# Optimization experiments

Measured on AMD Instinct MI355X. Metric: run time of the kernel, lower is better.

The kernel has to match this reference:

```python
import jax, jax.numpy as jnp
import numpy as np

NUM_EMBEDDINGS = 1024
EMBEDDING_SIZE = 256
COMMITMENT_COST = 0.25


def setup_inputs() -> dict:
    key = jax.random.key(0)
    kx, kw = jax.random.split(key)
    x = jax.random.normal(kx, (16, EMBEDDING_SIZE, 64, 64), dtype=jnp.float32)
    # nn.Embedding init: uniform(-1/K, 1/K)
    w = jax.random.uniform(kw, (NUM_EMBEDDINGS, EMBEDDING_SIZE), dtype=jnp.float32,
                           minval=-1.0 / NUM_EMBEDDINGS, maxval=1.0 / NUM_EMBEDDINGS)
    return {"x": x, "w": w}


def reference(x, w):
    # x: [B, C, H, W] -> NHWC
    xh = jnp.transpose(x, (0, 2, 3, 1))  # [B, H, W, D]
    B, H, W, D = xh.shape
    x_flat = xh.reshape(-1, D)  # [N, D]
    distances = (jnp.sum(x_flat * x_flat, axis=1, keepdims=True)
                 + jnp.sum(w * w, axis=1)
                 - 2.0 * (x_flat @ w.T))  # [N, K]
    indices_flat = jnp.argmin(distances, axis=1)  # [N]
    quantized = w[indices_flat].reshape(B, H, W, D)
    indices = indices_flat.reshape(B, H, W)[:, None, :, :]  # [B,1,H,W]
    # training-mode losses
    e_latent_loss = jnp.mean((jax.lax.stop_gradient(quantized) - xh) ** 2)
    q_latent_loss = jnp.mean((quantized - jax.lax.stop_gradient(xh)) ** 2)
    loss = q_latent_loss + COMMITMENT_COST * e_latent_loss
    # straight-through estimator
    quantized = xh + jax.lax.stop_gradient(quantized - xh)
    quantized = jnp.transpose(quantized, (0, 3, 1, 2))  # back to NCHW
    return quantized, indices, loss
```

## Files before the change

kernel.cpp:

```cpp
#include <hip/hip_runtime.h>
#include <math.h>

#define NUM_K 1024
#define DIM 256
#define HW 4096
#define NPIX 65536
#define QELEMS 16777216
#define MAX_FLAGS 16384

typedef short bf16x8 __attribute__((ext_vector_type(8)));
typedef float f32x4 __attribute__((ext_vector_type(4)));

__device__ __forceinline__ unsigned short f32_to_bf16_rne(float f) {
    unsigned int u = __float_as_uint(f);
    unsigned int r = u + 0x7FFFu + ((u >> 16) & 1u);
    return (unsigned short)(r >> 16);
}
__device__ __forceinline__ float bf16_to_f32(unsigned short h) {
    return __uint_as_float(((unsigned int)h) << 16);
}

__device__ __forceinline__ void merge3(float& a1d, int& a1i, float& a2d, int& a2i, float& a3d,
                                       float b1d, int b1i, float b2d, int b2i, float b3d) {
    bool bf = (b1d < a1d) || (b1d == a1d && b1i < a1i);
    float r1d = bf ? b1d : a1d; int r1i = bf ? b1i : a1i;
    float n2d = bf ? b2d : a2d; int n2i = bf ? b2i : a2i;
    float o1d = bf ? a1d : b1d; int o1i = bf ? a1i : b1i;
    bool k2 = (n2d < o1d) || (n2d == o1d && n2i < o1i);
    float r2d = k2 ? n2d : o1d; int r2i = k2 ? n2i : o1i;
    float sm3 = bf ? b3d : a3d;
    float o2d = bf ? a2d : b2d;
    float r3d = k2 ? fminf(sm3, o1d) : fminf(n2d, o2d);
    a1d = r1d; a1i = r1i; a2d = r2d; a2i = r2i; a3d = r3d;
}

__device__ __forceinline__ float np_sumsq_256(const float* __restrict__ p, long stride) {
    float blk0 = 0.f, blk1 = 0.f;
#pragma unroll
    for (int h = 0; h < 2; ++h) {
        const float* base = p + (long)h * 128 * stride;
        float s[16];
#pragma unroll
        for (int L = 0; L < 16; ++L) {
            float a0 = base[(long)(L)       * stride]; a0 = __fmul_rn(a0, a0);
            float a1 = base[(long)(16 + L)  * stride]; a1 = __fmul_rn(a1, a1);
            float a2 = base[(long)(32 + L)  * stride]; a2 = __fmul_rn(a2, a2);
            float a3 = base[(long)(48 + L)  * stride]; a3 = __fmul_rn(a3, a3);
            float a4 = base[(long)(64 + L)  * stride]; a4 = __fmul_rn(a4, a4);
            float a5 = base[(long)(80 + L)  * stride]; a5 = __fmul_rn(a5, a5);
            float a6 = base[(long)(96 + L)  * stride]; a6 = __fmul_rn(a6, a6);
            float a7 = base[(long)(112 + L) * stride]; a7 = __fmul_rn(a7, a7);
            float t1 = __fadd_rn(a0, a1);
            float t2 = __fadd_rn(a2, a3);
            float t3 = __fadd_rn(a4, a5);
            float t4 = __fadd_rn(a6, a7);
            s[L] = __fadd_rn(__fadd_rn(t1, t2), __fadd_rn(t3, t4));
        }
        float c0 = __fadd_rn(s[0], s[8]);
        float c1 = __fadd_rn(s[1], s[9]);
        float c2 = __fadd_rn(s[2], s[10]);
        float c3 = __fadd_rn(s[3], s[11]);
        float c4 = __fadd_rn(s[4], s[12]);
        float c5 = __fadd_rn(s[5], s[13]);
        float c6 = __fadd_rn(s[6], s[14]);
        float c7 = __fadd_rn(s[7], s[15]);
        float d0 = __fadd_rn(c0, c4);
        float d1 = __fadd_rn(c1, c5);
        float d2 = __fadd_rn(c2, c6);
        float d3 = __fadd_rn(c3, c7);
        float e0 = __fadd_rn(d0, d2);
        float e1 = __fadd_rn(d1, d3);
        float r  = __fadd_rn(e0, e1);
        if (h == 0) blk0 = r; else blk1 = r;
    }
    return __fadd_rn(blk0, blk1);
}

__global__ __launch_bounds__(256) void k_wsq(const float* __restrict__ w, float* __restrict__ wsq) {
    int k = blockIdx.x * 256 + threadIdx.x;
    if (k < NUM_K) wsq[k] = np_sumsq_256(w + (long)k * DIM, 1);
}

__global__ __launch_bounds__(256) void k_xsq(const float* __restrict__ x, float* __restrict__ xsq) {
    int n = blockIdx.x * 256 + threadIdx.x;
    int b = n >> 12, hw = n & 4095;
    xsq[n] = np_sumsq_256(x + (long)b * DIM * HW + hw, HW);
}

__global__ __launch_bounds__(1024)
void k_wtrans(const float* __restrict__ w, float* __restrict__ wtr) {
    int d = blockIdx.x;
    int k = threadIdx.x;
    wtr[(long)d * NUM_K + k] = w[(long)k * DIM + d];
}

__global__ __launch_bounds__(256)
void k_wfrag(const float* __restrict__ w, short* __restrict__ whi) {
    int id = blockIdx.x * 256 + threadIdx.x;
    int code = id >> 5;
    int c = id & 31;
    const float* src = w + (long)code * DIM + c * 8;
    bf16x8 vh;
#pragma unroll
    for (int j = 0; j < 8; ++j) vh[j] = (short)f32_to_bf16_rne(src[j]);
    int fl = ((c & 3) << 4) | (code & 15);
    long addr = ((((long)(code >> 4) * 8 + (c >> 2)) * 64 + fl) * 8);
    *(bf16x8*)(whi + addr) = vh;
}

#define A_SLOT(ks,m,fl) ((((ks)*4+(m))*64+(fl))*8)

__global__ __launch_bounds__(256, 2)
void k_argmin_mfma(const float* __restrict__ x,
                   const short* __restrict__ whi,
                   const float* __restrict__ wsq, const float* __restrict__ xsq,
                   float* __restrict__ pd1, int* __restrict__ pi1,
                   float* __restrict__ pd2, int* __restrict__ pi2,
                   float* __restrict__ pd3) {
    __shared__ short ahi[8 * 4 * 64 * 8];
    __shared__ float cd1[4][64], cd2[4][64], cd3[4][64];
    __shared__ int   ci1[4][64], ci2[4][64];

    const int t = threadIdx.x;
    const int lane = t & 63;
    const int q = t >> 6;
    const int tile = blockIdx.x >> 1;
    const int slice = blockIdx.x & 1;

    const int b = tile >> 6;
    const int hw0 = (tile & 63) * 64;
    const float* xb = x + (long)b * (DIM * HW) + hw0 + lane;

#pragma unroll
    for (int i = 0; i < 8; ++i) {
        int c = q * 8 + i;
        float v[8];
#pragma unroll
        for (int jj = 0; jj < 8; ++jj) v[jj] = xb[(long)(c * 8 + jj) * HW];
        bf16x8 vh;
#pragma unroll
        for (int jj = 0; jj < 8; ++jj) vh[jj] = (short)f32_to_bf16_rne(v[jj]);
        int slot = A_SLOT(c >> 2, lane >> 4, ((c & 3) << 4) | (lane & 15));
        *(bf16x8*)(ahi + slot) = vh;
    }
    __syncthreads();

    const int ct0 = slice * 32 + q * 8;
    f32x4 acc[4][8];
#pragma unroll
    for (int m = 0; m < 4; ++m)
#pragma unroll
        for (int n = 0; n < 8; ++n) acc[m][n] = (f32x4){0.f, 0.f, 0.f, 0.f};

#define BADDR(i) ((((long)(ct0 + ((i) & 7)) * 8 + ((i) >> 3)) * 64 + lane) * 8)
    bf16x8 bring[4];
#pragma unroll
    for (int i = 0; i < 4; ++i) bring[i] = *(const bf16x8*)(whi + BADDR(i));

    bf16x8 ah[4];
#pragma unroll
    for (int i = 0; i < 64; ++i) {
        const int ks = i >> 3;
        const int n = i & 7;
        if (n == 0) {
#pragma unroll
            for (int m = 0; m < 4; ++m)
                ah[m] = *(const bf16x8*)(ahi + A_SLOT(ks, m, lane));
        }
        bf16x8 bcur = bring[i & 3];
        if (i + 4 < 64) bring[i & 3] = *(const bf16x8*)(whi + BADDR(i + 4));
#pragma unroll
        for (int m = 0; m < 4; ++m)
            acc[m][n] = __builtin_amdgcn_mfma_f32_16x16x32_bf16(ah[m], bcur, acc[m][n], 0, 0, 0);
    }
#undef BADDR

    const long px0 = (long)tile * 64;
    const int rbase = (lane >> 4) * 4;
    float s1v[4][4];
#pragma unroll
    for (int m = 0; m < 4; ++m)
#pragma unroll
        for (int r = 0; r < 4; ++r) s1v[m][r] = xsq[px0 + 16 * m + rbase + r];

    float e1d[4][4], e2d[4][4], e3d[4][4];
    int   e1i[4][4], e2i[4][4];
#pragma unroll
    for (int m = 0; m < 4; ++m)
#pragma unroll
        for (int r = 0; r < 4; ++r) {
            e1d[m][r] = INFINITY; e2d[m][r] = INFINITY; e3d[m][r] = INFINITY;
            e1i[m][r] = 0; e2i[m][r] = 0;
        }

#pragma unroll
    for (int n = 0; n < 8; ++n) {
        int code = (ct0 + n) * 16 + (lane & 15);
        float wq = wsq[code];
#pragma unroll
        for (int m = 0; m < 4; ++m) {
#pragma unroll
            for (int r = 0; r < 4; ++r) {
                float tt = __fadd_rn(s1v[m][r], wq);
                float dist = __fmaf_rn(-2.0f, acc[m][n][r], tt);
                bool c1 = dist < e1d[m][r];
                bool c2 = dist < e2d[m][r];
                bool c3 = dist < e3d[m][r];
                float n3 = c2 ? e2d[m][r] : (c3 ? dist : e3d[m][r]);
                float n2 = c1 ? e1d[m][r] : (c2 ? dist : e2d[m][r]);
                int   j2 = c1 ? e1i[m][r] : (c2 ? code : e2i[m][r]);
                float n1 = c1 ? dist : e1d[m][r];
                int   j1 = c1 ? code : e1i[m][r];
                e3d[m][r] = n3; e2d[m][r] = n2; e2i[m][r] = j2;
                e1d[m][r] = n1; e1i[m][r] = j1;
            }
        }
    }

#pragma unroll
    for (int step = 1; step < 16; step <<= 1) {
#pragma unroll
        for (int m = 0; m < 4; ++m) {
#pragma unroll
            for (int r = 0; r < 4; ++r) {
                float o1 = __shfl_xor(e1d[m][r], step);
                int   p1 = __shfl_xor(e1i[m][r], step);
                float o2 = __shfl_xor(e2d[m][r], step);
                int   p2 = __shfl_xor(e2i[m][r], step);
                float o3 = __shfl_xor(e3d[m][r], step);
                merge3(e1d[m][r], e1i[m][r], e2d[m][r], e2i[m][r], e3d[m][r],
                       o1, p1, o2, p2, o3);
            }
        }
    }

    if ((lane & 15) == 0) {
#pragma unroll
        for (int m = 0; m < 4; ++m) {
#pragma unroll
            for (int r = 0; r < 4; ++r) {
                int px = 16 * m + rbase + r;
                cd1[q][px] = e1d[m][r]; ci1[q][px] = e1i[m][r];
                cd2[q][px] = e2d[m][r]; ci2[q][px] = e2i[m][r];
                cd3[q][px] = e3d[m][r];
            }
        }
    }
    __syncthreads();

    if (t < 64) {
        float d1 = cd1[0][t], d2 = cd2[0][t], d3 = cd3[0][t];
        int   i1 = ci1[0][t], i2 = ci2[0][t];
#pragma unroll
        for (int s = 1; s < 4; ++s) {
            merge3(d1, i1, d2, i2, d3, cd1[s][t], ci1[s][t], cd2[s][t], ci2[s][t], cd3[s][t]);
        }
        long n = (long)slice * NPIX + px0 + t;
        pd1[n] = d1; pi1[n] = i1; pd2[n] = d2; pi2[n] = i2; pd3[n] = d3;
    }
}

__global__ __launch_bounds__(256)
void k_combine(const float* __restrict__ pd1, const int* __restrict__ pi1,
               const float* __restrict__ pd2, const int* __restrict__ pi2,
               const float* __restrict__ pd3, int* __restrict__ idx,
               int4* __restrict__ pairf, int* __restrict__ paircnt,
               int* __restrict__ fullf, int* __restrict__ fullcnt) {
    int n = blockIdx.x * 256 + threadIdx.x;
    float d1 = pd1[n], d2 = pd2[n], d3 = pd3[n];
    int   i1 = pi1[n], i2 = pi2[n];
    long n1 = (long)NPIX + n;
    merge3(d1, i1, d2, i2, d3, pd1[n1], pi1[n1], pd2[n1], pi2[n1], pd3[n1]);
    idx[n] = i1;
    float m = d1 * 2.5e-6f;
    if (__fsub_rn(d3, d1) <= m) {
        int pos = atomicAdd(fullcnt, 1);
        if (pos < MAX_FLAGS) fullf[pos] = n;
    } else if (__fsub_rn(d2, d1) <= m) {
        int pos = atomicAdd(paircnt, 1);
        if (pos < MAX_FLAGS) pairf[pos] = (int4){n, i1, i2, 0};
    }
}

__global__ __launch_bounds__(256, 2)
void k_argmin_valu(const float* __restrict__ x, const float* __restrict__ w,
                   const float* __restrict__ wsq, const float* __restrict__ xsq,
                   int* __restrict__ idx, int* __restrict__ fullf, int* __restrict__ fullcnt) {
    __shared__ float xs[64 * 257];
    __shared__ float sd1[4][64];
    __shared__ float sd2[4][64];
    __shared__ int   si1[4][64];

    const int t = threadIdx.x;
    const int p = t & 63;
    const int q = t >> 6;
    const long n0 = (long)blockIdx.x * 64;
    const int b = (int)(n0 >> 12);
    const int hw0 = (int)(n0 & 4095);
    const float* xb = x + (long)b * DIM * HW + hw0;

    for (int i = 0; i < 64; ++i) {
        int c = q * 64 + i;
        xs[p * 257 + c] = xb[(long)c * HW + p];
    }
    __syncthreads();

    const float* xrow = xs + p * 257;
    const float s1 = xsq[n0 + p];
    float d1 = INFINITY, d2 = INFINITY;
    int i1 = 0;
    const int kbase = q * 256;
    const float* wq = w + (long)kbase * DIM;
    const float* wsq_q = wsq + kbase;

    for (int kc = 0; kc < 256; kc += 8) {
        float acc[8] = {0.f, 0.f, 0.f, 0.f, 0.f, 0.f, 0.f, 0.f};
        const float* w0 = wq + (long)kc * DIM;
#pragma unroll 2
        for (int d = 0; d < DIM; d += 4) {
            float x0 = xrow[d + 0];
            float x1 = xrow[d + 1];
            float x2 = xrow[d + 2];
            float x3 = xrow[d + 3];
#pragma unroll
            for (int j = 0; j < 8; ++j) {
                const float4 wv = *reinterpret_cast<const float4*>(w0 + j * DIM + d);
                acc[j] = __fmaf_rn(x0, wv.x, acc[j]);
                acc[j] = __fmaf_rn(x1, wv.y, acc[j]);
                acc[j] = __fmaf_rn(x2, wv.z, acc[j]);
                acc[j] = __fmaf_rn(x3, wv.w, acc[j]);
            }
        }
#pragma unroll
        for (int j = 0; j < 8; ++j) {
            float tk = __fadd_rn(s1, wsq_q[kc + j]);
            float dist = __fsub_rn(tk, __fmul_rn(2.0f, acc[j]));
            if (dist < d1) { d2 = d1; d1 = dist; i1 = kbase + kc + j; }
            else if (dist < d2) { d2 = dist; }
        }
    }

    sd1[q][p] = d1; sd2[q][p] = d2; si1[q][p] = i1;
    __syncthreads();
    if (q == 0) {
        float bd1 = sd1[0][p], bd2 = sd2[0][p];
        int bi = si1[0][p];
#pragma unroll
        for (int j = 1; j < 4; ++j) {
            float a1 = sd1[j][p], a2 = sd2[j][p];
            int ai = si1[j][p];
            if (a1 < bd1) { bd2 = fminf(bd1, a2); bd1 = a1; bi = ai; }
            else { bd2 = fminf(bd2, fminf(a1, a2)); }
        }
        const long n = n0 + p;
        idx[n] = bi;
        if (__fsub_rn(bd2, bd1) <= bd1 * 6.0e-7f) {
            int pos = atomicAdd(fullcnt, 1);
            if (pos < MAX_FLAGS) fullf[pos] = (int)n;
        }
    }
}

__global__ __launch_bounds__(256)
void k_refine_pair(const float* __restrict__ x, const float* __restrict__ w,
                   const float* __restrict__ wsq, const float* __restrict__ xsq,
                   const int4* __restrict__ pairf, const int* __restrict__ paircnt,
                   int* __restrict__ idx) {
    int np = *paircnt;
    if (np > MAX_FLAGS) np = MAX_FLAGS;
    const int lane = threadIdx.x & 63;
    const int wv = threadIdx.x >> 6;
    for (int fi = blockIdx.x * 4 + wv; fi < np; fi += gridDim.x * 4) {
        int4 f = pairf[fi];
        int n = f.x, c1 = f.y, c2 = f.z;
        int b = n >> 12, hw = n & 4095;
        const float* xp = x + (long)b * (DIM * HW) + hw;
        double xd0 = (double)xp[(long)(lane * 4 + 0) * HW];
        double xd1 = (double)xp[(long)(lane * 4 + 1) * HW];
        double xd2 = (double)xp[(long)(lane * 4 + 2) * HW];
        double xd3 = (double)xp[(long)(lane * 4 + 3) * HW];
        const float4 w1 = *reinterpret_cast<const float4*>(w + (long)c1 * DIM + lane * 4);
        const float4 w2 = *reinterpret_cast<const float4*>(w + (long)c2 * DIM + lane * 4);
        double s1 = fma((double)w1.x, xd0, fma((double)w1.y, xd1,
                    fma((double)w1.z, xd2, (double)w1.w * xd3)));
        double s2 = fma((double)w2.x, xd0, fma((double)w2.y, xd1,
                    fma((double)w2.z, xd2, (double)w2.w * xd3)));
#pragma unroll
        for (int st = 1; st < 64; st <<= 1) {
            s1 += __shfl_xor(s1, st);
            s2 += __shfl_xor(s2, st);
        }
        if (lane == 0) {
            float xq = xsq[n];
            float dk1 = __fsub_rn(__fadd_rn(xq, wsq[c1]), __fmul_rn(2.0f, (float)s1));
            float dk2 = __fsub_rn(__fadd_rn(xq, wsq[c2]), __fmul_rn(2.0f, (float)s2));
            bool take2 = (dk2 < dk1) || (dk2 == dk1 && c2 < c1);
            idx[n] = take2 ? c2 : c1;
        }
    }
}

__global__ __launch_bounds__(1024)
void k_refine_full(const float* __restrict__ x, const float* __restrict__ wtr,
                   const float* __restrict__ wsq, const float* __restrict__ xsq,
                   const int* __restrict__ fullf, const int* __restrict__ fullcnt,
                   int* __restrict__ idx) {
    __shared__ float xsf[DIM][8];
    __shared__ int   np_s[8];
    __shared__ float s1_s[8];
    __shared__ float wd[16][8];
    __shared__ int   wi[16][8];

    int nf = *fullcnt;
    if (nf > MAX_FLAGS) nf = MAX_FLAGS;
    const int t = threadIdx.x;
    const int lane = t & 63;
    const int wid = t >> 6;

    for (int base = blockIdx.x * 8; base < nf; base += gridDim.x * 8) {
        __syncthreads();
        if (t < 8) {
            int fi = base + t;
            int n = fullf[fi < nf ? fi : (nf - 1)];
            np_s[t] = n;
            s1_s[t] = xsq[n];
        }
        __syncthreads();
#pragma unroll
        for (int e = t; e < 2048; e += 1024) {
            int p = e & 7, d = e >> 3;
            int n = np_s[p];
            xsf[d][p] = x[(long)(n >> 12) * (DIM * HW) + (long)d * HW + (n & 4095)];
        }
        __syncthreads();

        const float wq = wsq[t];
        double acc[8] = {0.0, 0.0, 0.0, 0.0, 0.0, 0.0, 0.0, 0.0};
#pragma unroll 4
        for (int d = 0; d < DIM; ++d) {
            double wk = (double)wtr[(long)d * NUM_K + t];
#pragma unroll
            for (int p = 0; p < 8; ++p) acc[p] = fma(wk, (double)xsf[d][p], acc[p]);
        }

        float dkv[8];
        int   kiv[8];
#pragma unroll
        for (int p = 0; p < 8; ++p) {
            dkv[p] = __fsub_rn(__fadd_rn(s1_s[p], wq), __fmul_rn(2.0f, (float)acc[p]));
            kiv[p] = t;
        }
#pragma unroll
        for (int step = 1; step < 64; step <<= 1) {
#pragma unroll
            for (int p = 0; p < 8; ++p) {
                float od = __shfl_xor(dkv[p], step);
                int   oi = __shfl_xor(kiv[p], step);
                if (od < dkv[p] || (od == dkv[p] && oi < kiv[p])) { dkv[p] = od; kiv[p] = oi; }
            }
        }
        if (lane == 0) {
#pragma unroll
            for (int p = 0; p < 8; ++p) { wd[wid][p] = dkv[p]; wi[wid][p] = kiv[p]; }
        }
        __syncthreads();
        if (t < 8) {
            float bd = wd[0][t];
            int   bi = wi[0][t];
#pragma unroll
            for (int s = 1; s < 16; ++s) {
                float ad = wd[s][t];
                int   ai = wi[s][t];
                if (ad < bd || (ad == bd && ai < bi)) { bd = ad; bi = ai; }
            }
            if (base + t < nf) idx[np_s[t]] = bi;
        }
    }
}

__global__ __launch_bounds__(256, 2)
void k_quant(const float* __restrict__ x, const float* __restrict__ w,
             const int* __restrict__ idx, float* __restrict__ qout,
             float* __restrict__ iout, float* __restrict__ loss) {
    __shared__ float wrow[64 * 257];
    __shared__ int lidx[64];
    __shared__ float part[4];
    const int t = threadIdx.x;
    const long n0 = (long)blockIdx.x * 64;
    const int b = (int)(n0 >> 12), hw0 = (int)(n0 & 4095);

    if (t < 64) lidx[t] = idx[n0 + t];
    __syncthreads();
    for (int i = 0; i < 64; ++i) {
        wrow[i * 257 + t] = w[(long)lidx[i] * DIM + t];
    }
    if (t < 64) iout[n0 + t] = (float)lidx[t];
    __syncthreads();

    const int p = t & 63, cg = t >> 6;
    const float* xb = x + (long)b * DIM * HW + hw0;
    float* qb = qout + (long)b * DIM * HW + hw0;
    float lsum = 0.f;
    for (int i = 0; i < 64; ++i) {
        int c = cg * 64 + i;
        float qv = wrow[p * 257 + c];
        long off = (long)c * HW + p;
        float xv = xb[off];
        float diff = __fsub_rn(qv, xv);
        qb[off] = __fadd_rn(xv, diff);
        lsum = __fmaf_rn(diff, diff, lsum);
    }
#pragma unroll
    for (int off = 32; off; off >>= 1) lsum += __shfl_down(lsum, off);
    if ((t & 63) == 0) part[t >> 6] = lsum;
    __syncthreads();
    if (t == 0) {
        float tot = (part[0] + part[1]) + (part[2] + part[3]);
        atomicAdd(loss, tot * (1.25f / 16777216.f));
    }
}

extern "C" void kernel_launch(void* const* d_in, const int* in_sizes, int n_in,
                              void* d_out, int out_size, void* d_ws, size_t ws_size,
                              hipStream_t stream) {
    const float* x = (const float*)d_in[0];
    const float* w = (const float*)d_in[1];

    float* qout = (float*)d_out;
    float* iout = qout + QELEMS;
    float* loss = iout + NPIX;

    char* wp = (char*)d_ws;
    int*   idx     = (int*)wp;      wp += (size_t)NPIX * 4;
    float* wsq     = (float*)wp;    wp += (size_t)NUM_K * 4;
    float* xsq     = (float*)wp;    wp += (size_t)NPIX * 4;
    int4*  pairf   = (int4*)wp;     wp += (size_t)MAX_FLAGS * 16;
    int*   paircnt = (int*)wp;      wp += 256;
    int*   fullf   = (int*)wp;      wp += (size_t)MAX_FLAGS * 4;
    int*   fullcnt = (int*)wp;      wp += 256;
    float* wtr     = (float*)wp;    wp += (size_t)NUM_K * DIM * 4;
    short* whi     = (short*)wp;    wp += (size_t)NUM_K * DIM * 2;
    float* pd1     = (float*)wp;    wp += (size_t)2 * NPIX * 4;
    int*   pi1     = (int*)wp;      wp += (size_t)2 * NPIX * 4;
    float* pd2     = (float*)wp;    wp += (size_t)2 * NPIX * 4;
    int*   pi2     = (int*)wp;      wp += (size_t)2 * NPIX * 4;
    float* pd3     = (float*)wp;    wp += (size_t)2 * NPIX * 4;
    size_t need = (size_t)(wp - (char*)d_ws);

    hipMemsetAsync(loss, 0, sizeof(float), stream);
    hipMemsetAsync(paircnt, 0, sizeof(int), stream);
    hipMemsetAsync(fullcnt, 0, sizeof(int), stream);

    k_wsq<<<4, 256, 0, stream>>>(w, wsq);
    k_xsq<<<NPIX / 256, 256, 0, stream>>>(x, xsq);
    k_wtrans<<<DIM, 1024, 0, stream>>>(w, wtr);

    if (ws_size >= need) {
        k_wfrag<<<128, 256, 0, stream>>>(w, whi);
        k_argmin_mfma<<<2048, 256, 0, stream>>>(x, whi, wsq, xsq, pd1, pi1, pd2, pi2, pd3);
        k_combine<<<NPIX / 256, 256, 0, stream>>>(pd1, pi1, pd2, pi2, pd3, idx,
                                                  pairf, paircnt, fullf, fullcnt);
        k_refine_pair<<<2048, 256, 0, stream>>>(x, w, wsq, xsq, pairf, paircnt, idx);
    } else {
        k_argmin_valu<<<NPIX / 64, 256, 0, stream>>>(x, w, wsq, xsq, idx, fullf, fullcnt);
    }
    k_refine_full<<<512, 1024, 0, stream>>>(x, wtr, wsq, xsq, fullf, fullcnt, idx);
    k_quant<<<NPIX / 64, 256, 0, stream>>>(x, w, idx, qout, iout, loss);
}
```

Measured before the change: 251.2 us.

## Fuse xsq, codebook-half combine and top-2 tracking into single MFMA argmin kernel

The MFMA argmin kernel now handles all 1024 codes per 64-pixel tile by looping over both halves, instead of splitting them across two blocks. It also computes the per-pixel squared norms while staging x, which removes the separate k_xsq pass, the partial-result buffers, k_combine and k_refine_pair. Top-3 tracking becomes top-2, and any near-tie goes straight to the full fp64-style refine. This saves launches and global traffic, but halves the grid, lengthens each block's work, and may send more pixels to the costly full refine.

```diff
diff --git a/kernel.cpp b/kernel.cpp
--- a/kernel.cpp
+++ b/kernel.cpp
@@ -15,23 +15,6 @@
     unsigned int u = __float_as_uint(f);
     unsigned int r = u + 0x7FFFu + ((u >> 16) & 1u);
     return (unsigned short)(r >> 16);
-}
-__device__ __forceinline__ float bf16_to_f32(unsigned short h) {
-    return __uint_as_float(((unsigned int)h) << 16);
-}
-
-__device__ __forceinline__ void merge3(float& a1d, int& a1i, float& a2d, int& a2i, float& a3d,
-                                       float b1d, int b1i, float b2d, int b2i, float b3d) {
-    bool bf = (b1d < a1d) || (b1d == a1d && b1i < a1i);
-    float r1d = bf ? b1d : a1d; int r1i = bf ? b1i : a1i;
-    float n2d = bf ? b2d : a2d; int n2i = bf ? b2i : a2i;
-    float o1d = bf ? a1d : b1d; int o1i = bf ? a1i : b1i;
-    bool k2 = (n2d < o1d) || (n2d == o1d && n2i < o1i);
-    float r2d = k2 ? n2d : o1d; int r2i = k2 ? n2i : o1i;
-    float sm3 = bf ? b3d : a3d;
-    float o2d = bf ? a2d : b2d;
-    float r3d = k2 ? fminf(sm3, o1d) : fminf(n2d, o2d);
-    a1d = r1d; a1i = r1i; a2d = r2d; a2i = r2i; a3d = r3d;
 }
 
 __device__ __forceinline__ float np_sumsq_256(const float* __restrict__ p, long stride) {
@@ -113,172 +96,209 @@
 __global__ __launch_bounds__(256, 2)
 void k_argmin_mfma(const float* __restrict__ x,
                    const short* __restrict__ whi,
-                   const float* __restrict__ wsq, const float* __restrict__ xsq,
-                   float* __restrict__ pd1, int* __restrict__ pi1,
-                   float* __restrict__ pd2, int* __restrict__ pi2,
-                   float* __restrict__ pd3) {
+                   const float* __restrict__ wsq, float* __restrict__ xsq,
+                   int* __restrict__ idx,
+                   int* __restrict__ fullf, int* __restrict__ fullcnt) {
     __shared__ short ahi[8 * 4 * 64 * 8];
-    __shared__ float cd1[4][64], cd2[4][64], cd3[4][64];
-    __shared__ int   ci1[4][64], ci2[4][64];
+    __shared__ float xpart[4 * 16 * 64];
+    __shared__ float xsq_s[64];
+    __shared__ float cd1[4][64], cd2[4][64];
+    __shared__ int   ci1[4][64];
 
     const int t = threadIdx.x;
     const int lane = t & 63;
     const int q = t >> 6;
-    const int tile = blockIdx.x >> 1;
-    const int slice = blockIdx.x & 1;
-
+    const int tile = blockIdx.x;
     const int b = tile >> 6;
     const int hw0 = (tile & 63) * 64;
+    const long px0 = (long)tile * 64;
     const float* xb = x + (long)b * (DIM * HW) + hw0 + lane;
 
-#pragma unroll
-    for (int i = 0; i < 8; ++i) {
-        int c = q * 8 + i;
-        float v[8];
-#pragma unroll
-        for (int jj = 0; jj < 8; ++jj) v[jj] = xb[(long)(c * 8 + jj) * HW];
-        bf16x8 vh;
-#pragma unroll
-        for (int jj = 0; jj < 8; ++jj) vh[jj] = (short)f32_to_bf16_rne(v[jj]);
-        int slot = A_SLOT(c >> 2, lane >> 4, ((c & 3) << 4) | (lane & 15));
-        *(bf16x8*)(ahi + slot) = vh;
-    }
-    __syncthreads();
-
-    const int ct0 = slice * 32 + q * 8;
-    f32x4 acc[4][8];
-#pragma unroll
-    for (int m = 0; m < 4; ++m)
-#pragma unroll
-        for (int n = 0; n < 8; ++n) acc[m][n] = (f32x4){0.f, 0.f, 0.f, 0.f};
+    {
+        float tmp[16], part[16];
+#pragma unroll
+        for (int i = 0; i < 8; ++i) {
+            int c = q * 8 + i;
+            float v[8];
+#pragma unroll
+            for (int jj = 0; jj < 8; ++jj) v[jj] = xb[(long)(c * 8 + jj) * HW];
+            bf16x8 vh;
+#pragma unroll
+            for (int jj = 0; jj < 8; ++jj) vh[jj] = (short)f32_to_bf16_rne(v[jj]);
+            int slot = A_SLOT(c >> 2, lane >> 4, ((c & 3) << 4) | (lane & 15));
+            *(bf16x8*)(ahi + slot) = vh;
+            const int kp = i >> 1;
+#pragma unroll
+            for (int jj = 0; jj < 8; ++jj) {
+                int L = ((i & 1) << 3) | jj;
+                float a = __fmul_rn(v[jj], v[jj]);
+                if (kp == 0) tmp[L] = a;
+                else if (kp == 1) part[L] = __fadd_rn(tmp[L], a);
+                else if (kp == 2) tmp[L] = a;
+                else part[L] = __fadd_rn(part[L], __fadd_rn(tmp[L], a));
+            }
+        }
+#pragma unroll
+        for (int L = 0; L < 16; ++L) xpart[(q * 16 + L) * 64 + lane] = part[L];
+    }
+    __syncthreads();
+
+    if (t < 64) {
+        float blk[2];
+#pragma unroll
+        for (int h = 0; h < 2; ++h) {
+            float s[16];
+#pragma unroll
+            for (int L = 0; L < 16; ++L)
+                s[L] = __fadd_rn(xpart[((2 * h) * 16 + L) * 64 + t],
+                                 xpart[((2 * h + 1) * 16 + L) * 64 + t]);
+            float c0 = __fadd_rn(s[0], s[8]);
+            float c1 = __fadd_rn(s[1], s[9]);
+            float c2 = __fadd_rn(s[2], s[10]);
+            float c3 = __fadd_rn(s[3], s[11]);
+            float c4 = __fadd_rn(s[4], s[12]);
+            float c5 = __fadd_rn(s[5], s[13]);
+            float c6 = __fadd_rn(s[6], s[14]);
+            float c7 = __fadd_rn(s[7], s[15]);
+            float d0 = __fadd_rn(c0, c4);
+            float d1 = __fadd_rn(c1, c5);
+            float d2 = __fadd_rn(c2, c6);
+            float d3 = __fadd_rn(c3, c7);
+            float e0 = __fadd_rn(d0, d2);
+            float e1 = __fadd_rn(d1, d3);
+            blk[h] = __fadd_rn(e0, e1);
+        }
+        float v = __fadd_rn(blk[0], blk[1]);
+        xsq_s[t] = v;
+        xsq[px0 + t] = v;
+    }
+    __syncthreads();
+
+#pragma unroll
+    for (int s = 0; s < 2; ++s) {
+        const int ct0 = s * 32 + q * 8;
+        f32x4 acc[4][8];
+#pragma unroll
+        for (int m = 0; m < 4; ++m)
+#pragma unroll
+            for (int n = 0; n < 8; ++n) acc[m][n] = (f32x4){0.f, 0.f, 0.f, 0.f};
 
 #define BADDR(i) ((((long)(ct0 + ((i) & 7)) * 8 + ((i) >> 3)) * 64 + lane) * 8)
-    bf16x8 bring[4];
-#pragma unroll
-    for (int i = 0; i < 4; ++i) bring[i] = *(const bf16x8*)(whi + BADDR(i));
-
-    bf16x8 ah[4];
-#pragma unroll
-    for (int i = 0; i < 64; ++i) {
-        const int ks = i >> 3;
-        const int n = i & 7;
-        if (n == 0) {
+        bf16x8 bring[4];
+#pragma unroll
+        for (int i = 0; i < 4; ++i) bring[i] = *(const bf16x8*)(whi + BADDR(i));
+
+        bf16x8 ah[4];
+#pragma unroll
+        for (int i = 0; i < 64; ++i) {
+            const int ks = i >> 3;
+            const int n = i & 7;
+            if (n == 0) {
+#pragma unroll
+                for (int m = 0; m < 4; ++m)
+                    ah[m] = *(const bf16x8*)(ahi + A_SLOT(ks, m, lane));
+            }
+            bf16x8 bcur = bring[i & 3];
+            if (i + 4 < 64) bring[i & 3] = *(const bf16x8*)(whi + BADDR(i + 4));
 #pragma unroll
             for (int m = 0; m < 4; ++m)
-                ah[m] = *(const bf16x8*)(ahi + A_SLOT(ks, m, lane));
-        }
-        bf16x8 bcur = bring[i & 3];
-        if (i + 4 < 64) bring[i & 3] = *(const bf16x8*)(whi + BADDR(i + 4));
+                acc[m][n] = __builtin_amdgcn_mfma_f32_16x16x32_bf16(ah[m], bcur, acc[m][n], 0, 0, 0);
+        }
+#undef BADDR
+
+        const int rbase = (lane >> 4) * 4;
+        float s1v[4][4];
 #pragma unroll
         for (int m = 0; m < 4; ++m)
-            acc[m][n] = __builtin_amdgcn_mfma_f32_16x16x32_bf16(ah[m], bcur, acc[m][n], 0, 0, 0);
-    }
-#undef BADDR
-
-    const long px0 = (long)tile * 64;
-    const int rbase = (lane >> 4) * 4;
-    float s1v[4][4];
-#pragma unroll
-    for (int m = 0; m < 4; ++m)
-#pragma unroll
-        for (int r = 0; r < 4; ++r) s1v[m][r] = xsq[px0 + 16 * m + rbase + r];
-
-    float e1d[4][4], e2d[4][4], e3d[4][4];
-    int   e1i[4][4], e2i[4][4];
-#pragma unroll
-    for (int m = 0; m < 4; ++m)
-#pragma unroll
-        for (int r = 0; r < 4; ++r) {
-            e1d[m][r] = INFINITY; e2d[m][r] = INFINITY; e3d[m][r] = INFINITY;
-            e1i[m][r] = 0; e2i[m][r] = 0;
-        }
-
-#pragma unroll
-    for (int n = 0; n < 8; ++n) {
-        int code = (ct0 + n) * 16 + (lane & 15);
-        float wq = wsq[code];
-#pragma unroll
-        for (int m = 0; m < 4; ++m) {
-#pragma unroll
-            for (int r = 0; r < 4; ++r) {
-                float tt = __fadd_rn(s1v[m][r], wq);
-                float dist = __fmaf_rn(-2.0f, acc[m][n][r], tt);
-                bool c1 = dist < e1d[m][r];
-                bool c2 = dist < e2d[m][r];
-                bool c3 = dist < e3d[m][r];
-                float n3 = c2 ? e2d[m][r] : (c3 ? dist : e3d[m][r]);
-                float n2 = c1 ? e1d[m][r] : (c2 ? dist : e2d[m][r]);
-                int   j2 = c1 ? e1i[m][r] : (c2 ? code : e2i[m][r]);
-                float n1 = c1 ? dist : e1d[m][r];
-                int   j1 = c1 ? code : e1i[m][r];
-                e3d[m][r] = n3; e2d[m][r] = n2; e2i[m][r] = j2;
-                e1d[m][r] = n1; e1i[m][r] = j1;
-            }
-        }
-    }
-
-#pragma unroll
-    for (int step = 1; step < 16; step <<= 1) {
-#pragma unroll
-        for (int m = 0; m < 4; ++m) {
-#pragma unroll
-            for (int r = 0; r < 4; ++r) {
-                float o1 = __shfl_xor(e1d[m][r], step);
-                int   p1 = __shfl_xor(e1i[m][r], step);
-                float o2 = __shfl_xor(e2d[m][r], step);
-                int   p2 = __shfl_xor(e2i[m][r], step);
-                float o3 = __shfl_xor(e3d[m][r], step);
-                merge3(e1d[m][r], e1i[m][r], e2d[m][r], e2i[m][r], e3d[m][r],
-                       o1, p1, o2, p2, o3);
-            }
-        }
-    }
-
-    if ((lane & 15) == 0) {
-#pragma unroll
-        for (int m = 0; m < 4; ++m) {
-#pragma unroll
-            for (int r = 0; r < 4; ++r) {
-                int px = 16 * m + rbase + r;
-                cd1[q][px] = e1d[m][r]; ci1[q][px] = e1i[m][r];
-                cd2[q][px] = e2d[m][r]; ci2[q][px] = e2i[m][r];
-                cd3[q][px] = e3d[m][r];
+#pragma unroll
+            for (int r = 0; r < 4; ++r) s1v[m][r] = xsq_s[16 * m + rbase + r];
+
+        float e1d[4][4], e2d[4][4];
+        int   e1i[4][4];
+#pragma unroll
+        for (int m = 0; m < 4; ++m)
+#pragma unroll
+            for (int r = 0; r < 4; ++r) { e1d[m][r] = INFINITY; e2d[m][r] = INFINITY; e1i[m][r] = 0; }
+
+#pragma unroll
+        for (int n = 0; n < 8; ++n) {
+            int code = (ct0 + n) * 16 + (lane & 15);
+            float wq = wsq[code];
+#pragma unroll
+            for (int m = 0; m < 4; ++m) {
+#pragma unroll
+                for (int r = 0; r < 4; ++r) {
+                    float tt = __fadd_rn(s1v[m][r], wq);
+                    float dist = __fmaf_rn(-2.0f, acc[m][n][r], tt);
+                    bool c1 = dist < e1d[m][r];
+                    bool c2 = dist < e2d[m][r];
+                    e2d[m][r] = c1 ? e1d[m][r] : (c2 ? dist : e2d[m][r]);
+                    e1i[m][r] = c1 ? code : e1i[m][r];
+                    e1d[m][r] = c1 ? dist : e1d[m][r];
+                }
+            }
+        }
+
+#pragma unroll
+        for (int step = 1; step < 16; step <<= 1) {
+#pragma unroll
+            for (int m = 0; m < 4; ++m) {
+#pragma unroll
+                for (int r = 0; r < 4; ++r) {
+                    float o1 = __shfl_xor(e1d[m][r], step);
+                    int   oi = __shfl_xor(e1i[m][r], step);
+                    float o2 = __shfl_xor(e2d[m][r], step);
+                    bool take = (o1 < e1d[m][r]) || (o1 == e1d[m][r] && oi < e1i[m][r]);
+                    float nd2 = fminf(take ? e1d[m][r] : o1, take ? o2 : e2d[m][r]);
+                    e1d[m][r] = take ? o1 : e1d[m][r];
+                    e1i[m][r] = take ? oi : e1i[m][r];
+                    e2d[m][r] = nd2;
+                }
+            }
+        }
+
+        if ((lane & 15) == 0) {
+#pragma unroll
+            for (int m = 0; m < 4; ++m) {
+#pragma unroll
+                for (int r = 0; r < 4; ++r) {
+                    int px = 16 * m + rbase + r;
+                    if (s == 0) {
+                        cd1[q][px] = e1d[m][r]; ci1[q][px] = e1i[m][r]; cd2[q][px] = e2d[m][r];
+                    } else {
+                        float a1 = cd1[q][px], a2 = cd2[q][px];
+                        int   ai = ci1[q][px];
+                        bool take = (e1d[m][r] < a1) || (e1d[m][r] == a1 && e1i[m][r] < ai);
+                        float nd2 = fminf(take ? a1 : e1d[m][r], take ? e2d[m][r] : a2);
+                        cd1[q][px] = take ? e1d[m][r] : a1;
+                        ci1[q][px] = take ? e1i[m][r] : ai;
+                        cd2[q][px] = nd2;
+                    }
+                }
             }
         }
     }
     __syncthreads();
 
     if (t < 64) {
-        float d1 = cd1[0][t], d2 = cd2[0][t], d3 = cd3[0][t];
-        int   i1 = ci1[0][t], i2 = ci2[0][t];
-#pragma unroll
-        for (int s = 1; s < 4; ++s) {
-            merge3(d1, i1, d2, i2, d3, cd1[s][t], ci1[s][t], cd2[s][t], ci2[s][t], cd3[s][t]);
-        }
-        long n = (long)slice * NPIX + px0 + t;
-        pd1[n] = d1; pi1[n] = i1; pd2[n] = d2; pi2[n] = i2; pd3[n] = d3;
-    }
-}
-
-__global__ __launch_bounds__(256)
-void k_combine(const float* __restrict__ pd1, const int* __restrict__ pi1,
-               const float* __restrict__ pd2, const int* __restrict__ pi2,
-               const float* __restrict__ pd3, int* __restrict__ idx,
-               int4* __restrict__ pairf, int* __restrict__ paircnt,
-               int* __restrict__ fullf, int* __restrict__ fullcnt) {
-    int n = blockIdx.x * 256 + threadIdx.x;
-    float d1 = pd1[n], d2 = pd2[n], d3 = pd3[n];
-    int   i1 = pi1[n], i2 = pi2[n];
-    long n1 = (long)NPIX + n;
-    merge3(d1, i1, d2, i2, d3, pd1[n1], pi1[n1], pd2[n1], pi2[n1], pd3[n1]);
-    idx[n] = i1;
-    float m = d1 * 2.5e-6f;
-    if (__fsub_rn(d3, d1) <= m) {
-        int pos = atomicAdd(fullcnt, 1);
-        if (pos < MAX_FLAGS) fullf[pos] = n;
-    } else if (__fsub_rn(d2, d1) <= m) {
-        int pos = atomicAdd(paircnt, 1);
-        if (pos < MAX_FLAGS) pairf[pos] = (int4){n, i1, i2, 0};
+        float d1 = cd1[0][t], d2 = cd2[0][t];
+        int   i1 = ci1[0][t];
+#pragma unroll
+        for (int sq = 1; sq < 4; ++sq) {
+            float a1 = cd1[sq][t], a2 = cd2[sq][t];
+            int   ai = ci1[sq][t];
+            bool take = (a1 < d1) || (a1 == d1 && ai < i1);
+            float nd2 = fminf(take ? d1 : a1, take ? a2 : d2);
+            d1 = take ? a1 : d1;
+            i1 = take ? ai : i1;
+            d2 = nd2;
+        }
+        const long n = px0 + t;
+        idx[n] = i1;
+        if (__fsub_rn(d2, d1) <= d1 * 2.5e-6f) {
+            int pos = atomicAdd(fullcnt, 1);
+            if (pos < MAX_FLAGS) fullf[pos] = (int)n;
+        }
     }
 }
 
@@ -357,45 +377,6 @@
         if (__fsub_rn(bd2, bd1) <= bd1 * 6.0e-7f) {
             int pos = atomicAdd(fullcnt, 1);
             if (pos < MAX_FLAGS) fullf[pos] = (int)n;
-        }
-    }
-}
-
-__global__ __launch_bounds__(256)
-void k_refine_pair(const float* __restrict__ x, const float* __restrict__ w,
-                   const float* __restrict__ wsq, const float* __restrict__ xsq,
-                   const int4* __restrict__ pairf, const int* __restrict__ paircnt,
-                   int* __restrict__ idx) {
-    int np = *paircnt;
-    if (np > MAX_FLAGS) np = MAX_FLAGS;
-    const int lane = threadIdx.x & 63;
-    const int wv = threadIdx.x >> 6;
-    for (int fi = blockIdx.x * 4 + wv; fi < np; fi += gridDim.x * 4) {
-        int4 f = pairf[fi];
-        int n = f.x, c1 = f.y, c2 = f.z;
-        int b = n >> 12, hw = n & 4095;
-        const float* xp = x + (long)b * (DIM * HW) + hw;
-        double xd0 = (double)xp[(long)(lane * 4 + 0) * HW];
-        double xd1 = (double)xp[(long)(lane * 4 + 1) * HW];
-        double xd2 = (double)xp[(long)(lane * 4 + 2) * HW];
-        double xd3 = (double)xp[(long)(lane * 4 + 3) * HW];
-        const float4 w1 = *reinterpret_cast<const float4*>(w + (long)c1 * DIM + lane * 4);
-        const float4 w2 = *reinterpret_cast<const float4*>(w + (long)c2 * DIM + lane * 4);
-        double s1 = fma((double)w1.x, xd0, fma((double)w1.y, xd1,
-                    fma((double)w1.z, xd2, (double)w1.w * xd3)));
-        double s2 = fma((double)w2.x, xd0, fma((double)w2.y, xd1,
-                    fma((double)w2.z, xd2, (double)w2.w * xd3)));
-#pragma unroll
-        for (int st = 1; st < 64; st <<= 1) {
-            s1 += __shfl_xor(s1, st);
-            s2 += __shfl_xor(s2, st);
-        }
-        if (lane == 0) {
-            float xq = xsq[n];
-            float dk1 = __fsub_rn(__fadd_rn(xq, wsq[c1]), __fmul_rn(2.0f, (float)s1));
-            float dk2 = __fsub_rn(__fadd_rn(xq, wsq[c2]), __fmul_rn(2.0f, (float)s2));
-            bool take2 = (dk2 < dk1) || (dk2 == dk1 && c2 < c1);
-            idx[n] = take2 ? c2 : c1;
         }
     }
 }
@@ -468,9 +449,9 @@
             float bd = wd[0][t];
             int   bi = wi[0][t];
 #pragma unroll
-            for (int s = 1; s < 16; ++s) {
-                float ad = wd[s][t];
-                int   ai = wi[s][t];
+            for (int sq = 1; sq < 16; ++sq) {
+                float ad = wd[sq][t];
+                int   ai = wi[sq][t];
                 if (ad < bd || (ad == bd && ai < bi)) { bd = ad; bi = ai; }
             }
             if (base + t < nf) idx[np_s[t]] = bi;
@@ -534,34 +515,23 @@
     int*   idx     = (int*)wp;      wp += (size_t)NPIX * 4;
     float* wsq     = (float*)wp;    wp += (size_t)NUM_K * 4;
     float* xsq     = (float*)wp;    wp += (size_t)NPIX * 4;
-    int4*  pairf   = (int4*)wp;     wp += (size_t)MAX_FLAGS * 16;
-    int*   paircnt = (int*)wp;      wp += 256;
     int*   fullf   = (int*)wp;      wp += (size_t)MAX_FLAGS * 4;
     int*   fullcnt = (int*)wp;      wp += 256;
     float* wtr     = (float*)wp;    wp += (size_t)NUM_K * DIM * 4;
     short* whi     = (short*)wp;    wp += (size_t)NUM_K * DIM * 2;
-    float* pd1     = (float*)wp;    wp += (size_t)2 * NPIX * 4;
-    int*   pi1     = (int*)wp;      wp += (size_t)2 * NPIX * 4;
-    float* pd2     = (float*)wp;    wp += (size_t)2 * NPIX * 4;
-    int*   pi2     = (int*)wp;      wp += (size_t)2 * NPIX * 4;
-    float* pd3     = (float*)wp;    wp += (size_t)2 * NPIX * 4;
     size_t need = (size_t)(wp - (char*)d_ws);
 
     hipMemsetAsync(loss, 0, sizeof(float), stream);
-    hipMemsetAsync(paircnt, 0, sizeof(int), stream);
     hipMemsetAsync(fullcnt, 0, sizeof(int), stream);
 
     k_wsq<<<4, 256, 0, stream>>>(w, wsq);
-    k_xsq<<<NPIX / 256, 256, 0, stream>>>(x, xsq);
     k_wtrans<<<DIM, 1024, 0, stream>>>(w, wtr);
 
     if (ws_size >= need) {
         k_wfrag<<<128, 256, 0, stream>>>(w, whi);
-        k_argmin_mfma<<<2048, 256, 0, stream>>>(x, whi, wsq, xsq, pd1, pi1, pd2, pi2, pd3);
-        k_combine<<<NPIX / 256, 256, 0, stream>>>(pd1, pi1, pd2, pi2, pd3, idx,
-                                                  pairf, paircnt, fullf, fullcnt);
-        k_refine_pair<<<2048, 256, 0, stream>>>(x, w, wsq, xsq, pairf, paircnt, idx);
+        k_argmin_mfma<<<1024, 256, 0, stream>>>(x, whi, wsq, xsq, idx, fullf, fullcnt);
     } else {
+        k_xsq<<<NPIX / 256, 256, 0, stream>>>(x, xsq);
         k_argmin_valu<<<NPIX / 64, 256, 0, stream>>>(x, w, wsq, xsq, idx, fullf, fullcnt);
     }
     k_refine_full<<<512, 1024, 0, stream>>>(x, wtr, wsq, xsq, fullf, fullcnt, idx);
```

New measurement: 339.3 us. 1.35x slower.

## Fuse xsq and combine into MFMA argmin, one block per tile covering both halves

Applied to the files above, without the earlier changes.

The MFMA argmin kernel now computes per-pixel squared norms from the x values it already loads, which removes the separate xsq pass over x. Each block loops over both codebook halves itself and merges the top-3 candidates in shared memory, so the partial-result buffers and the combine kernel go away. The grid halves to 1024 blocks, which cuts parallelism and leaves each block with a longer serial MFMA loop. The xsq summation order is written out by hand so it stays identical to the old kernel's.

```diff
diff --git a/kernel.cpp b/kernel.cpp
--- a/kernel.cpp
+++ b/kernel.cpp
@@ -15,9 +15,6 @@
     unsigned int u = __float_as_uint(f);
     unsigned int r = u + 0x7FFFu + ((u >> 16) & 1u);
     return (unsigned short)(r >> 16);
-}
-__device__ __forceinline__ float bf16_to_f32(unsigned short h) {
-    return __uint_as_float(((unsigned int)h) << 16);
 }
 
 __device__ __forceinline__ void merge3(float& a1d, int& a1i, float& a2d, int& a2i, float& a3d,
@@ -113,136 +110,195 @@
 __global__ __launch_bounds__(256, 2)
 void k_argmin_mfma(const float* __restrict__ x,
                    const short* __restrict__ whi,
-                   const float* __restrict__ wsq, const float* __restrict__ xsq,
-                   float* __restrict__ pd1, int* __restrict__ pi1,
-                   float* __restrict__ pd2, int* __restrict__ pi2,
-                   float* __restrict__ pd3) {
+                   const float* __restrict__ wsq, float* __restrict__ xsq,
+                   int* __restrict__ idx,
+                   int4* __restrict__ pairf, int* __restrict__ paircnt,
+                   int* __restrict__ fullf, int* __restrict__ fullcnt) {
     __shared__ short ahi[8 * 4 * 64 * 8];
+    __shared__ float xpart[4 * 16 * 64];
+    __shared__ float xsq_s[64];
     __shared__ float cd1[4][64], cd2[4][64], cd3[4][64];
     __shared__ int   ci1[4][64], ci2[4][64];
 
     const int t = threadIdx.x;
     const int lane = t & 63;
     const int q = t >> 6;
-    const int tile = blockIdx.x >> 1;
-    const int slice = blockIdx.x & 1;
-
+    const int tile = blockIdx.x;
     const int b = tile >> 6;
     const int hw0 = (tile & 63) * 64;
+    const long px0 = (long)tile * 64;
     const float* xb = x + (long)b * (DIM * HW) + hw0 + lane;
 
-#pragma unroll
-    for (int i = 0; i < 8; ++i) {
-        int c = q * 8 + i;
-        float v[8];
-#pragma unroll
-        for (int jj = 0; jj < 8; ++jj) v[jj] = xb[(long)(c * 8 + jj) * HW];
-        bf16x8 vh;
-#pragma unroll
-        for (int jj = 0; jj < 8; ++jj) vh[jj] = (short)f32_to_bf16_rne(v[jj]);
-        int slot = A_SLOT(c >> 2, lane >> 4, ((c & 3) << 4) | (lane & 15));
-        *(bf16x8*)(ahi + slot) = vh;
-    }
-    __syncthreads();
-
-    const int ct0 = slice * 32 + q * 8;
-    f32x4 acc[4][8];
-#pragma unroll
-    for (int m = 0; m < 4; ++m)
-#pragma unroll
-        for (int n = 0; n < 8; ++n) acc[m][n] = (f32x4){0.f, 0.f, 0.f, 0.f};
+    {
+        float tmp[16], part[16];
+#pragma unroll
+        for (int i = 0; i < 8; ++i) {
+            int c = q * 8 + i;
+            float v[8];
+#pragma unroll
+            for (int jj = 0; jj < 8; ++jj) v[jj] = xb[(long)(c * 8 + jj) * HW];
+            bf16x8 vh;
+#pragma unroll
+            for (int jj = 0; jj < 8; ++jj) vh[jj] = (short)f32_to_bf16_rne(v[jj]);
+            int slot = A_SLOT(c >> 2, lane >> 4, ((c & 3) << 4) | (lane & 15));
+            *(bf16x8*)(ahi + slot) = vh;
+            const int kp = i >> 1;
+#pragma unroll
+            for (int jj = 0; jj < 8; ++jj) {
+                int L = ((i & 1) << 3) | jj;
+                float a = __fmul_rn(v[jj], v[jj]);
+                if (kp == 0) tmp[L] = a;
+                else if (kp == 1) part[L] = __fadd_rn(tmp[L], a);
+                else if (kp == 2) tmp[L] = a;
+                else part[L] = __fadd_rn(part[L], __fadd_rn(tmp[L], a));
+            }
+        }
+#pragma unroll
+        for (int L = 0; L < 16; ++L) xpart[(q * 16 + L) * 64 + lane] = part[L];
+    }
+    __syncthreads();
+
+    if (t < 64) {
+        float blk[2];
+#pragma unroll
+        for (int h = 0; h < 2; ++h) {
+            float s[16];
+#pragma unroll
+            for (int L = 0; L < 16; ++L)
+                s[L] = __fadd_rn(xpart[((2 * h) * 16 + L) * 64 + t],
+                                 xpart[((2 * h + 1) * 16 + L) * 64 + t]);
+            float c0 = __fadd_rn(s[0], s[8]);
+            float c1 = __fadd_rn(s[1], s[9]);
+            float c2 = __fadd_rn(s[2], s[10]);
+            float c3 = __fadd_rn(s[3], s[11]);
+            float c4 = __fadd_rn(s[4], s[12]);
+            float c5 = __fadd_rn(s[5], s[13]);
+            float c6 = __fadd_rn(s[6], s[14]);
+            float c7 = __fadd_rn(s[7], s[15]);
+            float d0 = __fadd_rn(c0, c4);
+            float d1 = __fadd_rn(c1, c5);
+            float d2 = __fadd_rn(c2, c6);
+            float d3 = __fadd_rn(c3, c7);
+            float e0 = __fadd_rn(d0, d2);
+            float e1 = __fadd_rn(d1, d3);
+            blk[h] = __fadd_rn(e0, e1);
+        }
+        float v = __fadd_rn(blk[0], blk[1]);
+        xsq_s[t] = v;
+        xsq[px0 + t] = v;
+    }
+    __syncthreads();
+
+#pragma unroll
+    for (int s = 0; s < 2; ++s) {
+        const int ct0 = s * 32 + q * 8;
+        f32x4 acc[4][8];
+#pragma unroll
+        for (int m = 0; m < 4; ++m)
+#pragma unroll
+            for (int n = 0; n < 8; ++n) acc[m][n] = (f32x4){0.f, 0.f, 0.f, 0.f};
 
 #define BADDR(i) ((((long)(ct0 + ((i) & 7)) * 8 + ((i) >> 3)) * 64 + lane) * 8)
-    bf16x8 bring[4];
-#pragma unroll
-    for (int i = 0; i < 4; ++i) bring[i] = *(const bf16x8*)(whi + BADDR(i));
-
-    bf16x8 ah[4];
-#pragma unroll
-    for (int i = 0; i < 64; ++i) {
-        const int ks = i >> 3;
-        const int n = i & 7;
-        if (n == 0) {
+        bf16x8 bring[4];
+#pragma unroll
+        for (int i = 0; i < 4; ++i) bring[i] = *(const bf16x8*)(whi + BADDR(i));
+
+        bf16x8 ah[4];
+#pragma unroll
+        for (int i = 0; i < 64; ++i) {
+            const int ks = i >> 3;
+            const int n = i & 7;
+            if (n == 0) {
+#pragma unroll
+                for (int m = 0; m < 4; ++m)
+                    ah[m] = *(const bf16x8*)(ahi + A_SLOT(ks, m, lane));
+            }
+            bf16x8 bcur = bring[i & 3];
+            if (i + 4 < 64) bring[i & 3] = *(const bf16x8*)(whi + BADDR(i + 4));
 #pragma unroll
             for (int m = 0; m < 4; ++m)
-                ah[m] = *(const bf16x8*)(ahi + A_SLOT(ks, m, lane));
-        }
-        bf16x8 bcur = bring[i & 3];
-        if (i + 4 < 64) bring[i & 3] = *(const bf16x8*)(whi + BADDR(i + 4));
+                acc[m][n] = __builtin_amdgcn_mfma_f32_16x16x32_bf16(ah[m], bcur, acc[m][n], 0, 0, 0);
+        }
+#undef BADDR
+
+        const int rbase = (lane >> 4) * 4;
+        float s1v[4][4];
 #pragma unroll
         for (int m = 0; m < 4; ++m)
-            acc[m][n] = __builtin_amdgcn_mfma_f32_16x16x32_bf16(ah[m], bcur, acc[m][n], 0, 0, 0);
-    }
-#undef BADDR
-
-    const long px0 = (long)tile * 64;
-    const int rbase = (lane >> 4) * 4;
-    float s1v[4][4];
-#pragma unroll
-    for (int m = 0; m < 4; ++m)
-#pragma unroll
-        for (int r = 0; r < 4; ++r) s1v[m][r] = xsq[px0 + 16 * m + rbase + r];
-
-    float e1d[4][4], e2d[4][4], e3d[4][4];
-    int   e1i[4][4], e2i[4][4];
-#pragma unroll
-    for (int m = 0; m < 4; ++m)
-#pragma unroll
-        for (int r = 0; r < 4; ++r) {
-            e1d[m][r] = INFINITY; e2d[m][r] = INFINITY; e3d[m][r] = INFINITY;
-            e1i[m][r] = 0; e2i[m][r] = 0;
-        }
-
-#pragma unroll
-    for (int n = 0; n < 8; ++n) {
-        int code = (ct0 + n) * 16 + (lane & 15);
-        float wq = wsq[code];
-#pragma unroll
-        for (int m = 0; m < 4; ++m) {
+#pragma unroll
+            for (int r = 0; r < 4; ++r) s1v[m][r] = xsq_s[16 * m + rbase + r];
+
+        float e1d[4][4], e2d[4][4], e3d[4][4];
+        int   e1i[4][4], e2i[4][4];
+#pragma unroll
+        for (int m = 0; m < 4; ++m)
 #pragma unroll
             for (int r = 0; r < 4; ++r) {
-                float tt = __fadd_rn(s1v[m][r], wq);
-                float dist = __fmaf_rn(-2.0f, acc[m][n][r], tt);
-                bool c1 = dist < e1d[m][r];
-                bool c2 = dist < e2d[m][r];
-                bool c3 = dist < e3d[m][r];
-                float n3 = c2 ? e2d[m][r] : (c3 ? dist : e3d[m][r]);
-                float n2 = c1 ? e1d[m][r] : (c2 ? dist : e2d[m][r]);
-                int   j2 = c1 ? e1i[m][r] : (c2 ? code : e2i[m][r]);
-                float n1 = c1 ? dist : e1d[m][r];
-                int   j1 = c1 ? code : e1i[m][r];
-                e3d[m][r] = n3; e2d[m][r] = n2; e2i[m][r] = j2;
-                e1d[m][r] = n1; e1i[m][r] = j1;
-            }
-        }
-    }
-
-#pragma unroll
-    for (int step = 1; step < 16; step <<= 1) {
-#pragma unroll
-        for (int m = 0; m < 4; ++m) {
-#pragma unroll
-            for (int r = 0; r < 4; ++r) {
-                float o1 = __shfl_xor(e1d[m][r], step);
-                int   p1 = __shfl_xor(e1i[m][r], step);
-                float o2 = __shfl_xor(e2d[m][r], step);
-                int   p2 = __shfl_xor(e2i[m][r], step);
-                float o3 = __shfl_xor(e3d[m][r], step);
-                merge3(e1d[m][r], e1i[m][r], e2d[m][r], e2i[m][r], e3d[m][r],
-                       o1, p1, o2, p2, o3);
-            }
-        }
-    }
-
-    if ((lane & 15) == 0) {
-#pragma unroll
-        for (int m = 0; m < 4; ++m) {
-#pragma unroll
-            for (int r = 0; r < 4; ++r) {
-                int px = 16 * m + rbase + r;
-                cd1[q][px] = e1d[m][r]; ci1[q][px] = e1i[m][r];
-                cd2[q][px] = e2d[m][r]; ci2[q][px] = e2i[m][r];
-                cd3[q][px] = e3d[m][r];
+                e1d[m][r] = INFINITY; e2d[m][r] = INFINITY; e3d[m][r] = INFINITY;
+                e1i[m][r] = 0; e2i[m][r] = 0;
+            }
+
+#pragma unroll
+        for (int n = 0; n < 8; ++n) {
+            int code = (ct0 + n) * 16 + (lane & 15);
+            float wq = wsq[code];
+#pragma unroll
+            for (int m = 0; m < 4; ++m) {
+#pragma unroll
+                for (int r = 0; r < 4; ++r) {
+                    float tt = __fadd_rn(s1v[m][r], wq);
+                    float dist = __fmaf_rn(-2.0f, acc[m][n][r], tt);
+                    bool c1 = dist < e1d[m][r];
+                    bool c2 = dist < e2d[m][r];
+                    bool c3 = dist < e3d[m][r];
+                    float n3 = c2 ? e2d[m][r] : (c3 ? dist : e3d[m][r]);
+                    float n2 = c1 ? e1d[m][r] : (c2 ? dist : e2d[m][r]);
+                    int   j2 = c1 ? e1i[m][r] : (c2 ? code : e2i[m][r]);
+                    float n1 = c1 ? dist : e1d[m][r];
+                    int   j1 = c1 ? code : e1i[m][r];
+                    e3d[m][r] = n3; e2d[m][r] = n2; e2i[m][r] = j2;
+                    e1d[m][r] = n1; e1i[m][r] = j1;
+                }
+            }
+        }
+
+#pragma unroll
+        for (int step = 1; step < 16; step <<= 1) {
+#pragma unroll
+            for (int m = 0; m < 4; ++m) {
+#pragma unroll
+                for (int r = 0; r < 4; ++r) {
+                    float o1 = __shfl_xor(e1d[m][r], step);
+                    int   p1 = __shfl_xor(e1i[m][r], step);
+                    float o2 = __shfl_xor(e2d[m][r], step);
+                    int   p2 = __shfl_xor(e2i[m][r], step);
+                    float o3 = __shfl_xor(e3d[m][r], step);
+                    merge3(e1d[m][r], e1i[m][r], e2d[m][r], e2i[m][r], e3d[m][r],
+                           o1, p1, o2, p2, o3);
+                }
+            }
+        }
+
+        if ((lane & 15) == 0) {
+#pragma unroll
+            for (int m = 0; m < 4; ++m) {
+#pragma unroll
+                for (int r = 0; r < 4; ++r) {
+                    int px = 16 * m + rbase + r;
+                    if (s == 0) {
+                        cd1[q][px] = e1d[m][r]; ci1[q][px] = e1i[m][r];
+                        cd2[q][px] = e2d[m][r]; ci2[q][px] = e2i[m][r];
+                        cd3[q][px] = e3d[m][r];
+                    } else {
+                        float a1 = cd1[q][px], a2 = cd2[q][px], a3 = cd3[q][px];
+                        int   ai = ci1[q][px], aj = ci2[q][px];
+                        merge3(a1, ai, a2, aj, a3,
+                               e1d[m][r], e1i[m][r], e2d[m][r], e2i[m][r], e3d[m][r]);
+                        cd1[q][px] = a1; ci1[q][px] = ai;
+                        cd2[q][px] = a2; ci2[q][px] = aj;
+                        cd3[q][px] = a3;
+                    }
+                }
             }
         }
     }
@@ -252,33 +308,20 @@
         float d1 = cd1[0][t], d2 = cd2[0][t], d3 = cd3[0][t];
         int   i1 = ci1[0][t], i2 = ci2[0][t];
 #pragma unroll
-        for (int s = 1; s < 4; ++s) {
-            merge3(d1, i1, d2, i2, d3, cd1[s][t], ci1[s][t], cd2[s][t], ci2[s][t], cd3[s][t]);
-        }
-        long n = (long)slice * NPIX + px0 + t;
-        pd1[n] = d1; pi1[n] = i1; pd2[n] = d2; pi2[n] = i2; pd3[n] = d3;
-    }
-}
-
-__global__ __launch_bounds__(256)
-void k_combine(const float* __restrict__ pd1, const int* __restrict__ pi1,
-               const float* __restrict__ pd2, const int* __restrict__ pi2,
-               const float* __restrict__ pd3, int* __restrict__ idx,
-               int4* __restrict__ pairf, int* __restrict__ paircnt,
-               int* __restrict__ fullf, int* __restrict__ fullcnt) {
-    int n = blockIdx.x * 256 + threadIdx.x;
-    float d1 = pd1[n], d2 = pd2[n], d3 = pd3[n];
-    int   i1 = pi1[n], i2 = pi2[n];
-    long n1 = (long)NPIX + n;
-    merge3(d1, i1, d2, i2, d3, pd1[n1], pi1[n1], pd2[n1], pi2[n1], pd3[n1]);
-    idx[n] = i1;
-    float m = d1 * 2.5e-6f;
-    if (__fsub_rn(d3, d1) <= m) {
-        int pos = atomicAdd(fullcnt, 1);
-        if (pos < MAX_FLAGS) fullf[pos] = n;
-    } else if (__fsub_rn(d2, d1) <= m) {
-        int pos = atomicAdd(paircnt, 1);
-        if (pos < MAX_FLAGS) pairf[pos] = (int4){n, i1, i2, 0};
+        for (int sq = 1; sq < 4; ++sq) {
+            merge3(d1, i1, d2, i2, d3,
+                   cd1[sq][t], ci1[sq][t], cd2[sq][t], ci2[sq][t], cd3[sq][t]);
+        }
+        const long n = px0 + t;
+        idx[n] = i1;
+        float m = d1 * 2.5e-6f;
+        if (__fsub_rn(d3, d1) <= m) {
+            int pos = atomicAdd(fullcnt, 1);
+            if (pos < MAX_FLAGS) fullf[pos] = (int)n;
+        } else if (__fsub_rn(d2, d1) <= m) {
+            int pos = atomicAdd(paircnt, 1);
+            if (pos < MAX_FLAGS) pairf[pos] = (int4){(int)n, i1, i2, 0};
+        }
     }
 }
 
@@ -468,9 +511,9 @@
             float bd = wd[0][t];
             int   bi = wi[0][t];
 #pragma unroll
-            for (int s = 1; s < 16; ++s) {
-                float ad = wd[s][t];
-                int   ai = wi[s][t];
+            for (int sq = 1; sq < 16; ++sq) {
+                float ad = wd[sq][t];
+                int   ai = wi[sq][t];
                 if (ad < bd || (ad == bd && ai < bi)) { bd = ad; bi = ai; }
             }
             if (base + t < nf) idx[np_s[t]] = bi;
@@ -540,11 +583,6 @@
     int*   fullcnt = (int*)wp;      wp += 256;
     float* wtr     = (float*)wp;    wp += (size_t)NUM_K * DIM * 4;
     short* whi     = (short*)wp;    wp += (size_t)NUM_K * DIM * 2;
-    float* pd1     = (float*)wp;    wp += (size_t)2 * NPIX * 4;
-    int*   pi1     = (int*)wp;      wp += (size_t)2 * NPIX * 4;
-    float* pd2     = (float*)wp;    wp += (size_t)2 * NPIX * 4;
-    int*   pi2     = (int*)wp;      wp += (size_t)2 * NPIX * 4;
-    float* pd3     = (float*)wp;    wp += (size_t)2 * NPIX * 4;
     size_t need = (size_t)(wp - (char*)d_ws);
 
     hipMemsetAsync(loss, 0, sizeof(float), stream);
@@ -552,16 +590,15 @@
     hipMemsetAsync(fullcnt, 0, sizeof(int), stream);
 
     k_wsq<<<4, 256, 0, stream>>>(w, wsq);
-    k_xsq<<<NPIX / 256, 256, 0, stream>>>(x, xsq);
     k_wtrans<<<DIM, 1024, 0, stream>>>(w, wtr);
 
     if (ws_size >= need) {
         k_wfrag<<<128, 256, 0, stream>>>(w, whi);
-        k_argmin_mfma<<<2048, 256, 0, stream>>>(x, whi, wsq, xsq, pd1, pi1, pd2, pi2, pd3);
-        k_combine<<<NPIX / 256, 256, 0, stream>>>(pd1, pi1, pd2, pi2, pd3, idx,
-                                                  pairf, paircnt, fullf, fullcnt);
+        k_argmin_mfma<<<1024, 256, 0, stream>>>(x, whi, wsq, xsq, idx,
+                                                pairf, paircnt, fullf, fullcnt);
         k_refine_pair<<<2048, 256, 0, stream>>>(x, w, wsq, xsq, pairf, paircnt, idx);
     } else {
+        k_xsq<<<NPIX / 256, 256, 0, stream>>>(x, xsq);
         k_argmin_valu<<<NPIX / 64, 256, 0, stream>>>(x, w, wsq, xsq, idx, fullf, fullcnt);
     }
     k_refine_full<<<512, 1024, 0, stream>>>(x, wtr, wsq, xsq, fullf, fullcnt, idx);
```

Result: faster. 239.7 us (-4.6%).
